# Optimization experiments

Hardware: AMD Instinct MI355X
Metric: run time of the kernel (lower is better)

The kernel has to match this reference:

```python
import jax, jax.numpy as jnp
import numpy as np

K = 1024  # codebook size
D = 256   # embedding dim


def setup_inputs() -> dict:
    key = jax.random.key(0)
    k1, k2 = jax.random.split(key)
    z_e_x = jax.random.normal(k1, (32, D, 32, 32), dtype=jnp.float32)  # NCHW
    # nn.Embedding weight initialized uniform(-1/K, 1/K)
    W = jax.random.uniform(k2, (K, D), dtype=jnp.float32, minval=-1.0 / K, maxval=1.0 / K)
    return {"z_e_x": z_e_x, "W": W}


def reference(z_e_x, W):
    # permute NCHW -> NHWC, flatten spatial, nearest-codebook lookup (vq)
    z = jnp.transpose(z_e_x, (0, 2, 3, 1))            # [B, H, Wd, D]
    B, H, Wd, Dd = z.shape
    flat = z.reshape(-1, Dd)                           # [N, D]
    # squared L2 distances: ||z||^2 - 2 z.W^T + ||W||^2
    z_sq = jnp.sum(flat * flat, axis=1, keepdims=True)         # [N, 1]
    w_sq = jnp.sum(W * W, axis=1)                               # [K]
    dists = z_sq - 2.0 * (flat @ W.T) + w_sq[None, :]           # [N, K]
    idx = jnp.argmin(dists, axis=1)                             # [N]
    latents = idx.reshape(B, H, Wd)                             # [B, H, Wd] int indices
    return latents
```

## Files before the change

kernel.cpp:

```cpp
#include <hip/hip_runtime.h>

#define NPOS 32768
#define DDIM 256
#define KCODES 1024

typedef __attribute__((ext_vector_type(8))) short bf16x8;
typedef __attribute__((ext_vector_type(4))) float f32x4;
typedef unsigned long long u64;

__device__ __forceinline__ float sqr_rn(float x) {
    float r = x * x;
    asm volatile("" : "+v"(r));
    return r;
}
__device__ __forceinline__ float add_rn(float a, float b) {
    float r = a + b;
    asm volatile("" : "+v"(r));
    return r;
}

__device__ __forceinline__ unsigned short f2bf(float x) {
    unsigned u = __float_as_uint(x);
    return (unsigned short)((u + 0x7fffu + ((u >> 16) & 1u)) >> 16);
}

__device__ __forceinline__ u64 packm(float s, int code) {
    unsigned b = __float_as_uint(s);
    unsigned mm = ((unsigned)((int)b >> 31)) | 0x80000000u;
    return ((u64)(b ^ mm) << 32) | (unsigned)code;
}

__device__ __forceinline__ void gld16(const void* g, void* lds) {
    __builtin_amdgcn_global_load_lds(
        (const __attribute__((address_space(1))) unsigned int*)g,
        (__attribute__((address_space(3))) unsigned int*)lds, 16, 0, 0);
}

__global__ __launch_bounds__(256) void zprep(const float* __restrict__ z,
                                             float* __restrict__ zsq,
                                             unsigned short* __restrict__ zb16) {
    __shared__ float part[4][64];
    __shared__ unsigned short Lb[256 * 65];

    const int t  = threadIdx.x;
    const int hw = t & 63;
    const int q  = t >> 6;
    const int m0 = blockIdx.x * 64;
    const int h  = q >> 1;
    const int cb = (q & 1) * 4;
    const float* zimg = z + (m0 >> 10) * (DDIM * 1024) + (m0 & 1023) + hw;

    float v[4][16];
#pragma unroll
    for (int c = 0; c < 4; ++c)
#pragma unroll
        for (int i = 0; i < 16; ++i)
            v[c][i] = zimg[(h * 128 + cb + c + 8 * i) * 1024];

    float r[4];
#pragma unroll
    for (int c = 0; c < 4; ++c) {
        r[c] = sqr_rn(v[c][0]);
#pragma unroll
        for (int i = 1; i < 16; ++i) r[c] = add_rn(r[c], sqr_rn(v[c][i]));
    }
    part[q][hw] = add_rn(add_rn(r[0], r[1]), add_rn(r[2], r[3]));

#pragma unroll
    for (int c = 0; c < 4; ++c)
#pragma unroll
        for (int i = 0; i < 16; ++i) {
            const int d = h * 128 + cb + c + 8 * i;
            Lb[d * 65 + hw] = f2bf(v[c][i]);
        }
    __syncthreads();
    if (t < 64)
        zsq[m0 + t] = add_rn(add_rn(part[0][t], part[1][t]),
                             add_rn(part[2][t], part[3][t]));
#pragma unroll
    for (int j = 0; j < 8; ++j) {
        const int c = t + j * 256;
        const int row = c >> 5, k8 = c & 31;
        bf16x8 o;
#pragma unroll
        for (int e = 0; e < 8; ++e) o[e] = (short)Lb[(k8 * 8 + e) * 65 + row];
        *(bf16x8*)&zb16[(m0 + row) * DDIM + k8 * 8] = o;
    }
}

__global__ __launch_bounds__(256) void wprep(const float* __restrict__ W,
                                             float* __restrict__ wsq,
                                             unsigned short* __restrict__ wb16) {
    const int t   = threadIdx.x;
    const int row = blockIdx.x * 16 + (t >> 4);
    const int j   = t & 15;
    const float* base = W + row * DDIM + (j & 7) + (j >> 3) * 128;
    float r = sqr_rn(base[0]);
#pragma unroll
    for (int i = 1; i < 16; ++i) r = add_rn(r, sqr_rn(base[i * 8]));
#pragma unroll
    for (int m = 1; m <= 8; m <<= 1) r = add_rn(r, __shfl_xor(r, m));
    if (j == 0) wsq[row] = r;

    const int e0 = blockIdx.x * 4096 + t * 16;
#pragma unroll
    for (int g = 0; g < 2; ++g) {
        const float4 f0 = *(const float4*)&W[e0 + g * 8];
        const float4 f1 = *(const float4*)&W[e0 + g * 8 + 4];
        bf16x8 o;
        o[0] = (short)f2bf(f0.x); o[1] = (short)f2bf(f0.y);
        o[2] = (short)f2bf(f0.z); o[3] = (short)f2bf(f0.w);
        o[4] = (short)f2bf(f1.x); o[5] = (short)f2bf(f1.y);
        o[6] = (short)f2bf(f1.z); o[7] = (short)f2bf(f1.w);
        *(bf16x8*)&wb16[e0 + g * 8] = o;
    }
}

__global__ __launch_bounds__(256) __attribute__((amdgpu_waves_per_eu(2, 2)))
void gemm_top2(const unsigned short* __restrict__ zb16,
               const unsigned short* __restrict__ wb16,
               const float* __restrict__ wsq, u64* __restrict__ cand) {
    __shared__ u64 redU[4096];
    char* Ab = (char*)redU;
    char* Bb = (char*)redU + 8192;

    const int t    = threadIdx.x;
    const int w    = t >> 6;
    const int l    = t & 63;
    const int ln   = l & 15;
    const int q    = l >> 4;
    const int mw   = (w & 1) * 64;
    const int nw   = (w >> 1) * 128;
    const int mblk = blockIdx.x >> 2;
    const int nblk = blockIdx.x & 3;
    const int m0   = mblk * 128;
    const int n0   = nblk * 256;

    const int am  = (w & 1) * 64 + l;
    const int akq = w >> 1;
    const char* gA0 = (const char*)(zb16 + (m0 + am) * DDIM) + akq * 16;
    const char* gB  = (const char*)(wb16 + (n0 + w * 64 + l) * DDIM);
    char* lA = Ab + w * 1024;
    char* lB = Bb + w * 1024;

    f32x4 acc[4][8];
#pragma unroll
    for (int a = 0; a < 4; ++a)
#pragma unroll
        for (int b = 0; b < 8; ++b) acc[a][b] = (f32x4)(0.f);

#pragma unroll 1
    for (int kk = 0; kk < 8; ++kk) {
        const int ko = kk * 64;
        gld16(gA0 + ko,      lA);
        gld16(gA0 + ko + 32, lA + 4096);
        gld16(gB + ko,       lB);
        gld16(gB + ko + 16,  lB + 4096);
        gld16(gB + ko + 32,  lB + 8192);
        gld16(gB + ko + 48,  lB + 12288);
        __syncthreads();
        bf16x8 afr[4];
#pragma unroll
        for (int mf = 0; mf < 4; ++mf)
            afr[mf] = *(const bf16x8*)(Ab + q * 2048 + (mw + mf * 16 + ln) * 16);
#pragma unroll
        for (int nf = 0; nf < 8; ++nf) {
            const bf16x8 bfr = *(const bf16x8*)(Bb + q * 4096 + (nw + nf * 16 + ln) * 16);
#pragma unroll
            for (int mf = 0; mf < 4; ++mf)
                acc[mf][nf] = __builtin_amdgcn_mfma_f32_16x16x32_bf16(
                    afr[mf], bfr, acc[mf][nf], 0, 0, 0);
        }
        __syncthreads();
    }

    float wq[8];
#pragma unroll
    for (int nf = 0; nf < 8; ++nf) wq[nf] = wsq[n0 + nw + nf * 16 + ln];

#pragma unroll
    for (int mf = 0; mf < 4; ++mf) {
#pragma unroll
        for (int reg = 0; reg < 4; ++reg) {
            const int row = mw + mf * 16 + q * 4 + reg;
            float s0 = 1e30f, s1 = 1e30f;
            int   i0 = 0,     i1 = 0;
#pragma unroll
            for (int nf = 0; nf < 8; ++nf) {
                const float s  = fmaf(-2.f, acc[mf][nf][reg], wq[nf]);
                const int   cc = n0 + nw + nf * 16 + ln;
                if (s < s0)      { s1 = s0; i1 = i0; s0 = s; i0 = cc; }
                else if (s < s1) { s1 = s; i1 = cc; }
            }
            u64 p0 = packm(s0, i0), p1 = packm(s1, i1);
            const u64 o0 = __shfl_xor(p0, 1);
            const u64 o1 = __shfl_xor(p1, 1);
            const u64 c0 = (p0 < o0) ? p0 : o0;
            const u64 hi = (p0 < o0) ? o0 : p0;
            const u64 lo = (p1 < o1) ? p1 : o1;
            const u64 c1 = (hi < lo) ? hi : lo;
            if ((ln & 1) == 0) {
                u64* slot = &redU[row * 32 + (w >> 1) * 16 + (ln >> 1) * 2];
                slot[0] = c0;
                slot[1] = c1;
            }
        }
    }
    __syncthreads();
    {
        const int r2 = t >> 1, half = t & 1;
        u64 c0 = ~0ull, c1 = ~0ull;
#pragma unroll
        for (int j = 0; j < 16; ++j) {
            const u64 v = redU[r2 * 32 + half * 16 + j];
            if (v < c0)      { c1 = c0; c0 = v; }
            else if (v < c1) { c1 = v; }
        }
        __syncthreads();
        redU[r2 * 4 + half * 2]     = c0;
        redU[r2 * 4 + half * 2 + 1] = c1;
    }
    __syncthreads();
    if (t < 128) {
        const u64 a = redU[t * 4], b = redU[t * 4 + 1];
        const u64 c = redU[t * 4 + 2], d = redU[t * 4 + 3];
        const u64 m1 = (a < c) ? a : c;
        const u64 hi = (a < c) ? c : a;
        const u64 lo = (b < d) ? b : d;
        const u64 m2 = (hi < lo) ? hi : lo;
        u64* o = &cand[(u64)(m0 + t) * 8 + nblk * 2];
        o[0] = m1;
        o[1] = m2;
    }
}

#define ZS 260
__global__ __launch_bounds__(256) void rescore(const float* __restrict__ z,
                                               const float* __restrict__ W,
                                               const float* __restrict__ zsq,
                                               const float* __restrict__ wsq,
                                               const u64* __restrict__ cand,
                                               int* __restrict__ out) {
    __shared__ float Zs[32 * ZS];
    const int t  = threadIdx.x;
    const int m0 = blockIdx.x * 32;
    const float* zimg = z + (m0 >> 10) * (DDIM * 1024) + (m0 & 1023);
#pragma unroll
    for (int j = 0; j < 8; ++j) {
        const int f4 = t + j * 256;
        const int d = f4 >> 3, p4 = f4 & 7;
        const float4 v = *(const float4*)&zimg[d * 1024 + p4 * 4];
        Zs[(p4 * 4 + 0) * ZS + d] = v.x;
        Zs[(p4 * 4 + 1) * ZS + d] = v.y;
        Zs[(p4 * 4 + 2) * ZS + d] = v.z;
        Zs[(p4 * 4 + 3) * ZS + d] = v.w;
    }
    __syncthreads();
    const int pl = t >> 3, slot = t & 7;
    const int p = m0 + pl;
    const int code = (int)(unsigned)(cand[(u64)p * 8 + slot] & 0xffffffffULL);
    const float* wr = W + code * DDIM;
    const float* zr = &Zs[pl * ZS];
    float M = 0.f;
#pragma unroll 8
    for (int d4 = 0; d4 < 64; ++d4) {
        const float4 zv = *(const float4*)&zr[d4 * 4];
        const float4 wv = *(const float4*)&wr[d4 * 4];
        M = fmaf(zv.x, wv.x, M);
        M = fmaf(zv.y, wv.y, M);
        M = fmaf(zv.z, wv.z, M);
        M = fmaf(zv.w, wv.w, M);
    }
    const float s = add_rn(fmaf(-2.f, M, zsq[p]), wsq[code]);
    u64 v = ((u64)__float_as_uint(s) << 32) | (unsigned)code;
#pragma unroll
    for (int m = 1; m <= 4; m <<= 1) {
        const u64 o = __shfl_xor(v, m);
        if (o < v) v = o;
    }
    if (slot == 0) out[p] = (int)(unsigned)(v & 0xffffffffULL);
}

extern "C" void kernel_launch(void* const* d_in, const int* in_sizes, int n_in,
                              void* d_out, int out_size, void* d_ws, size_t ws_size,
                              hipStream_t stream) {
    const float* z = (const float*)d_in[0];
    const float* W = (const float*)d_in[1];
    int* out = (int*)d_out;

    char* ws = (char*)d_ws;
    float*          zsq  = (float*)ws;
    float*          wsq  = (float*)(ws + 131072);
    u64*            cand = (u64*)(ws + 135168);
    unsigned short* zb16 = (unsigned short*)(ws + 2232320);
    unsigned short* wb16 = (unsigned short*)(ws + 19009536);

    wprep<<<KCODES / 16, 256, 0, stream>>>(W, wsq, wb16);
    zprep<<<NPOS / 64, 256, 0, stream>>>(z, zsq, zb16);
    gemm_top2<<<(NPOS / 128) * 4, 256, 0, stream>>>(zb16, wb16, wsq, cand);
    rescore<<<NPOS / 32, 256, 0, stream>>>(z, W, zsq, wsq, cand, out);
}
```

Measured before the change: 163.4 us.

## Pre-tile bf16 operands into GEMM tile layout and move z-norm into rescore

The z and W bf16 conversion kernels now write their outputs directly in the per-tile, per-k-chunk order that the GEMM loads into LDS. Each GEMM global-to-LDS load then becomes a contiguous 1 KB copy per wave instead of a strided row gather. The z prep kernel is simplified to coalesced float4 reads plus an 8-row transpose through LDS. The squared norm of z is dropped from that prep and recomputed inside rescore from the fp32 values already staged in shared memory, which removes a buffer and its traffic but adds some per-position arithmetic to rescore.

```diff
diff --git a/kernel.cpp b/kernel.cpp
--- a/kernel.cpp
+++ b/kernel.cpp
@@ -36,61 +36,35 @@
         (__attribute__((address_space(3))) unsigned int*)lds, 16, 0, 0);
 }
 
-__global__ __launch_bounds__(256) void zprep(const float* __restrict__ z,
-                                             float* __restrict__ zsq,
-                                             unsigned short* __restrict__ zb16) {
-    __shared__ float part[4][64];
-    __shared__ unsigned short Lb[256 * 65];
-
-    const int t  = threadIdx.x;
-    const int hw = t & 63;
-    const int q  = t >> 6;
-    const int m0 = blockIdx.x * 64;
-    const int h  = q >> 1;
-    const int cb = (q & 1) * 4;
-    const float* zimg = z + (m0 >> 10) * (DDIM * 1024) + (m0 & 1023) + hw;
-
-    float v[4][16];
-#pragma unroll
-    for (int c = 0; c < 4; ++c)
-#pragma unroll
-        for (int i = 0; i < 16; ++i)
-            v[c][i] = zimg[(h * 128 + cb + c + 8 * i) * 1024];
-
-    float r[4];
-#pragma unroll
-    for (int c = 0; c < 4; ++c) {
-        r[c] = sqr_rn(v[c][0]);
-#pragma unroll
-        for (int i = 1; i < 16; ++i) r[c] = add_rn(r[c], sqr_rn(v[c][i]));
-    }
-    part[q][hw] = add_rn(add_rn(r[0], r[1]), add_rn(r[2], r[3]));
-
-#pragma unroll
-    for (int c = 0; c < 4; ++c)
-#pragma unroll
-        for (int i = 0; i < 16; ++i) {
-            const int d = h * 128 + cb + c + 8 * i;
-            Lb[d * 65 + hw] = f2bf(v[c][i]);
-        }
-    __syncthreads();
-    if (t < 64)
-        zsq[m0 + t] = add_rn(add_rn(part[0][t], part[1][t]),
-                             add_rn(part[2][t], part[3][t]));
-#pragma unroll
-    for (int j = 0; j < 8; ++j) {
-        const int c = t + j * 256;
-        const int row = c >> 5, k8 = c & 31;
+__global__ __launch_bounds__(256) void zconv(const float* __restrict__ z,
+                                             unsigned short* __restrict__ zb16t) {
+    __shared__ unsigned short Ls[8 * 1024];
+    const int t   = threadIdx.x;
+    const int img = blockIdx.x >> 5;
+    const int dc  = blockIdx.x & 31;
+    const int kk  = dc >> 2, kq = dc & 3;
+    const float* zr = z + img * (DDIM * 1024) + dc * 8 * 1024;
+#pragma unroll
+    for (int e = 0; e < 8; ++e) {
+        const float4 v = *(const float4*)&zr[e * 1024 + t * 4];
+        unsigned short* o = &Ls[e * 1024 + t * 4];
+        o[0] = f2bf(v.x); o[1] = f2bf(v.y); o[2] = f2bf(v.z); o[3] = f2bf(v.w);
+    }
+    __syncthreads();
+#pragma unroll
+    for (int j = 0; j < 4; ++j) {
+        const int m = t + j * 256;
+        const int mtile = img * 8 + (m >> 7);
         bf16x8 o;
 #pragma unroll
-        for (int e = 0; e < 8; ++e) o[e] = (short)Lb[(k8 * 8 + e) * 65 + row];
-        *(bf16x8*)&zb16[(m0 + row) * DDIM + k8 * 8] = o;
+        for (int e = 0; e < 8; ++e) o[e] = (short)Ls[e * 1024 + m];
+        *(bf16x8*)&zb16t[mtile * 32768 + kk * 4096 + kq * 1024 + (m & 127) * 8] = o;
     }
 }
 
 __global__ __launch_bounds__(256) void wprep(const float* __restrict__ W,
                                              float* __restrict__ wsq,
-                                             unsigned short* __restrict__ wb16) {
+                                             unsigned short* __restrict__ wb16t) {
     const int t   = threadIdx.x;
     const int row = blockIdx.x * 16 + (t >> 4);
     const int j   = t & 15;
@@ -102,23 +76,26 @@
     for (int m = 1; m <= 8; m <<= 1) r = add_rn(r, __shfl_xor(r, m));
     if (j == 0) wsq[row] = r;
 
-    const int e0 = blockIdx.x * 4096 + t * 16;
-#pragma unroll
-    for (int g = 0; g < 2; ++g) {
-        const float4 f0 = *(const float4*)&W[e0 + g * 8];
-        const float4 f1 = *(const float4*)&W[e0 + g * 8 + 4];
+#pragma unroll
+    for (int jj = 0; jj < 2; ++jj) {
+        const int u  = t + jj * 256;
+        const int n  = blockIdx.x * 16 + (u >> 5);
+        const int k8 = u & 31;
+        const float4 f0 = *(const float4*)&W[n * DDIM + k8 * 8];
+        const float4 f1 = *(const float4*)&W[n * DDIM + k8 * 8 + 4];
         bf16x8 o;
         o[0] = (short)f2bf(f0.x); o[1] = (short)f2bf(f0.y);
         o[2] = (short)f2bf(f0.z); o[3] = (short)f2bf(f0.w);
         o[4] = (short)f2bf(f1.x); o[5] = (short)f2bf(f1.y);
         o[6] = (short)f2bf(f1.z); o[7] = (short)f2bf(f1.w);
-        *(bf16x8*)&wb16[e0 + g * 8] = o;
+        const int kk = k8 >> 2, kq = k8 & 3;
+        *(bf16x8*)&wb16t[(n >> 8) * 65536 + kk * 8192 + kq * 2048 + (n & 255) * 8] = o;
     }
 }
 
 __global__ __launch_bounds__(256) __attribute__((amdgpu_waves_per_eu(2, 2)))
-void gemm_top2(const unsigned short* __restrict__ zb16,
-               const unsigned short* __restrict__ wb16,
+void gemm_top2(const unsigned short* __restrict__ zb16t,
+               const unsigned short* __restrict__ wb16t,
                const float* __restrict__ wsq, u64* __restrict__ cand) {
     __shared__ u64 redU[4096];
     char* Ab = (char*)redU;
@@ -127,6 +104,7 @@
     const int t    = threadIdx.x;
     const int w    = t >> 6;
     const int l    = t & 63;
+    const int lg   = l * 16;
     const int ln   = l & 15;
     const int q    = l >> 4;
     const int mw   = (w & 1) * 64;
@@ -136,12 +114,8 @@
     const int m0   = mblk * 128;
     const int n0   = nblk * 256;
 
-    const int am  = (w & 1) * 64 + l;
-    const int akq = w >> 1;
-    const char* gA0 = (const char*)(zb16 + (m0 + am) * DDIM) + akq * 16;
-    const char* gB  = (const char*)(wb16 + (n0 + w * 64 + l) * DDIM);
-    char* lA = Ab + w * 1024;
-    char* lB = Bb + w * 1024;
+    const char* Az = (const char*)zb16t + (size_t)mblk * 65536;
+    const char* Bz = (const char*)wb16t + (size_t)nblk * 131072;
 
     f32x4 acc[4][8];
 #pragma unroll
@@ -151,13 +125,14 @@
 
 #pragma unroll 1
     for (int kk = 0; kk < 8; ++kk) {
-        const int ko = kk * 64;
-        gld16(gA0 + ko,      lA);
-        gld16(gA0 + ko + 32, lA + 4096);
-        gld16(gB + ko,       lB);
-        gld16(gB + ko + 16,  lB + 4096);
-        gld16(gB + ko + 32,  lB + 8192);
-        gld16(gB + ko + 48,  lB + 12288);
+        const char* a = Az + kk * 8192 + lg;
+        const char* b = Bz + kk * 16384 + lg;
+        gld16(a + w * 1024,        Ab + w * 1024);
+        gld16(a + (4 + w) * 1024,  Ab + (4 + w) * 1024);
+        gld16(b + w * 1024,        Bb + w * 1024);
+        gld16(b + (4 + w) * 1024,  Bb + (4 + w) * 1024);
+        gld16(b + (8 + w) * 1024,  Bb + (8 + w) * 1024);
+        gld16(b + (12 + w) * 1024, Bb + (12 + w) * 1024);
         __syncthreads();
         bf16x8 afr[4];
 #pragma unroll
@@ -237,7 +212,6 @@
 #define ZS 260
 __global__ __launch_bounds__(256) void rescore(const float* __restrict__ z,
                                                const float* __restrict__ W,
-                                               const float* __restrict__ zsq,
                                                const float* __restrict__ wsq,
                                                const u64* __restrict__ cand,
                                                int* __restrict__ out) {
@@ -258,9 +232,24 @@
     __syncthreads();
     const int pl = t >> 3, slot = t & 7;
     const int p = m0 + pl;
+    const float* zr = &Zs[pl * ZS];
+
+    float h0 = sqr_rn(zr[slot]);
+    float h1 = sqr_rn(zr[128 + slot]);
+#pragma unroll
+    for (int i = 1; i < 16; ++i) {
+        h0 = add_rn(h0, sqr_rn(zr[slot + 8 * i]));
+        h1 = add_rn(h1, sqr_rn(zr[128 + slot + 8 * i]));
+    }
+#pragma unroll
+    for (int m = 1; m <= 4; m <<= 1) {
+        h0 = add_rn(h0, __shfl_xor(h0, m));
+        h1 = add_rn(h1, __shfl_xor(h1, m));
+    }
+    const float zq = add_rn(h0, h1);
+
     const int code = (int)(unsigned)(cand[(u64)p * 8 + slot] & 0xffffffffULL);
     const float* wr = W + code * DDIM;
-    const float* zr = &Zs[pl * ZS];
     float M = 0.f;
 #pragma unroll 8
     for (int d4 = 0; d4 < 64; ++d4) {
@@ -271,7 +260,7 @@
         M = fmaf(zv.z, wv.z, M);
         M = fmaf(zv.w, wv.w, M);
     }
-    const float s = add_rn(fmaf(-2.f, M, zsq[p]), wsq[code]);
+    const float s = add_rn(fmaf(-2.f, M, zq), wsq[code]);
     u64 v = ((u64)__float_as_uint(s) << 32) | (unsigned)code;
 #pragma unroll
     for (int m = 1; m <= 4; m <<= 1) {
@@ -289,14 +278,13 @@
     int* out = (int*)d_out;
 
     char* ws = (char*)d_ws;
-    float*          zsq  = (float*)ws;
-    float*          wsq  = (float*)(ws + 131072);
-    u64*            cand = (u64*)(ws + 135168);
-    unsigned short* zb16 = (unsigned short*)(ws + 2232320);
-    unsigned short* wb16 = (unsigned short*)(ws + 19009536);
-
-    wprep<<<KCODES / 16, 256, 0, stream>>>(W, wsq, wb16);
-    zprep<<<NPOS / 64, 256, 0, stream>>>(z, zsq, zb16);
-    gemm_top2<<<(NPOS / 128) * 4, 256, 0, stream>>>(zb16, wb16, wsq, cand);
-    rescore<<<NPOS / 32, 256, 0, stream>>>(z, W, zsq, wsq, cand, out);
-}
+    float*          wsq   = (float*)ws;
+    u64*            cand  = (u64*)(ws + 4096);
+    unsigned short* zb16t = (unsigned short*)(ws + 2101248);
+    unsigned short* wb16t = (unsigned short*)(ws + 18878464);
+
+    wprep<<<KCODES / 16, 256, 0, stream>>>(W, wsq, wb16t);
+    zconv<<<32 * 32, 256, 0, stream>>>(z, zb16t);
+    gemm_top2<<<(NPOS / 128) * 4, 256, 0, stream>>>(zb16t, wb16t, wsq, cand);
+    rescore<<<NPOS / 32, 256, 0, stream>>>(z, W, wsq, cand, out);
+}
```

Result: faster. 149.0 us (-8.8%).
